# Performance work log

Hardware: AMD Instinct MI355X
Metric: run time of the kernel (lower is better)

The kernel has to match this reference:

```python
import jax, jax.numpy as jnp
import numpy as np

B, N, S = 32, 1000, 200
D, H, DK, FF, NL = 128, 8, 16, 512, 3
HK = H * DK


def _mha(x, Wq, Wk, Wv, Wo, bo):
    # x: [B, L, D]; manual multi-head attention matching the torch code
    Bv, L, _ = x.shape
    q = (x @ Wq).reshape(Bv, L, H, DK).transpose(0, 2, 1, 3)  # [B,H,L,dk]
    k = (x @ Wk).reshape(Bv, L, H, DK).transpose(0, 2, 1, 3)
    v = (x @ Wv).reshape(Bv, L, H, DK).transpose(0, 2, 1, 3)
    score = jnp.einsum('bhid,bhjd->bhij', q, k) / jnp.sqrt(jnp.asarray(DK, x.dtype))
    w = jax.nn.softmax(score, axis=-1)
    o = jnp.einsum('bhij,bhjd->bhid', w, v).transpose(0, 2, 1, 3).reshape(Bv, L, HK)
    return o @ Wo + bo


def _decoder_layer(x, Wq, Wk, Wv, Wo, bo, W1, b1, W2, b2):
    out1 = x + _mha(x, Wq, Wk, Wv, Wo, bo)
    ff = jax.nn.relu(out1 @ W1 + b1) @ W2 + b2
    return out1 + ff


def _forward(data, attention_bias, Wfirst, bfirst, Wlast, blast,
             Wq, Wk, Wv, Wo, bo, W1, b1, W2, b2, Wfin, bfin, sel):
    Bv, Np, Dm = data.shape
    Sn = sel.shape[1]
    bidx = jnp.arange(Bv)
    # _get_new_data: ordered list of unselected node indices, shape [B, N-S]
    mask = jnp.zeros((Bv, Np), bool).at[bidx[:, None], sel].set(True)
    vals = jnp.where(mask, Np, jnp.arange(Np)[None, :])
    unselect = jnp.sort(vals, axis=1)[:, : Np - Sn]            # [B, N-S]
    left = jnp.take_along_axis(data, unselect[:, :, None], axis=1)  # [B, N-S, D]
    # _get_encoding for first / last selected node
    first = data[bidx, sel[:, 0]]
    last = data[bidx, sel[:, -1]]
    ef = first @ Wfirst + bfirst
    el = last @ Wlast + blast
    out = jnp.concatenate([ef[:, None], left, el[:, None]], axis=1)  # [B, N-S+2, D]
    for i in range(Wq.shape[0]):
        out = _decoder_layer(out, Wq[i], Wk[i], Wv[i], Wo[i], bo[i],
                             W1[i], b1[i], W2[i], b2[i])
    logits = (out @ Wfin + bfin)[..., 0]                       # [B, N-S+2]
    # attention bias of current (last selected) node, gathered at unselected
    ab_cur = attention_bias[bidx, sel[:, -1]]                  # [B, N]
    ab_uns = jnp.take_along_axis(ab_cur, unselect, axis=1)     # [B, N-S]
    logits = logits.at[:, 1:-1].add(ab_uns)
    L = logits.shape[1]
    pos = jnp.arange(L)
    end_mask = (pos == 0) | (pos == L - 1)
    logits = jnp.where(end_mask[None, :], -jnp.inf, logits)
    props = jax.nn.softmax(logits, axis=-1)[:, 1:-1]           # [B, N-S]
    props = jnp.where(props <= 1e-5, props + 1e-7, props)
    # scatter back: selected positions -> -2, unselected -> props
    new_props = jnp.full((Bv, Np), -2.0, dtype=data.dtype)
    new_props = new_props.at[bidx[:, None], unselect].set(props)
    return new_props


def setup_inputs() -> dict:
    key = jax.random.key(0)
    ks = jax.random.split(key, 24)
    data = jax.random.normal(ks[0], (B, N, D), jnp.float32)
    # selected_node_list must contain unique indices per row (partial tour)
    sel = jax.vmap(lambda k: jax.random.permutation(k, N))(
        jax.random.split(ks[1], B))[:, :S].astype(jnp.int32)
    attention_bias = jax.random.normal(ks[2], (B, N, N), jnp.float32)

    def lin(k, shape, fan_in):
        return jax.random.normal(k, shape, jnp.float32) / np.float32(np.sqrt(fan_in))

    return dict(
        data=data,
        attention_bias=attention_bias,
        Wfirst=lin(ks[3], (D, D), D), bfirst=jnp.zeros((D,), jnp.float32),
        Wlast=lin(ks[4], (D, D), D), blast=jnp.zeros((D,), jnp.float32),
        Wq=lin(ks[5], (NL, D, HK), D),
        Wk=lin(ks[6], (NL, D, HK), D),
        Wv=lin(ks[7], (NL, D, HK), D),
        Wo=lin(ks[8], (NL, HK, D), HK), bo=jnp.zeros((NL, D), jnp.float32),
        W1=lin(ks[9], (NL, D, FF), D), b1=jnp.zeros((NL, FF), jnp.float32),
        W2=lin(ks[10], (NL, FF, D), FF), b2=jnp.zeros((NL, D), jnp.float32),
        Wfin=lin(ks[11], (D, 1), D), bfin=jnp.zeros((1,), jnp.float32),
        selected_node_list=sel,
    )


def reference(data, attention_bias, Wfirst, bfirst, Wlast, blast,
              Wq, Wk, Wv, Wo, bo, W1, b1, W2, b2, Wfin, bfin,
              selected_node_list):
    return _forward(data, attention_bias, Wfirst, bfirst, Wlast, blast,
                    Wq, Wk, Wv, Wo, bo, W1, b1, W2, b2, Wfin, bfin,
                    selected_node_list)
```

## Files before the change

kernel.cpp:

```cpp
#include <hip/hip_runtime.h>
#include <hip/hip_bf16.h>
#include <math.h>

#define NB 32
#define NN 1000
#define SS 200
#define DD 128
#define HH 8
#define DKK 16
#define FFD 512
#define NLAYER 3
#define LQ 802
#define LPAD 832
#define NPADK (LPAD - LQ)
#define MROWS (NB*LQ)
#define NBLK64 (MROWS/64)
#define NQT 26
#define NQT64 13
#define HSTR 516
#define TSTR 132
#define QSCALE 0.3606737602f

typedef __attribute__((ext_vector_type(8))) short short8;
typedef __attribute__((ext_vector_type(4))) short short4v;
typedef __attribute__((ext_vector_type(16))) float f32x16;
typedef __attribute__((ext_vector_type(2))) unsigned int uint2v;

static __device__ __forceinline__ unsigned short f2bf(float x) {
  union { float f; unsigned int u; } v; v.f = x;
  unsigned int r = v.u + 0x7fff + ((v.u >> 16) & 1);
  return (unsigned short)(r >> 16);
}

static __device__ __forceinline__ unsigned short f2bf1(float x) {
  unsigned int r;
  asm("v_cvt_pk_bf16_f32 %0, %1, 0" : "=v"(r) : "v"(x));
  return (unsigned short)r;
}

static __device__ __forceinline__ unsigned int cvtpk_bf16(float lo, float hi) {
  unsigned int r;
  asm("v_cvt_pk_bf16_f32 %0, %1, %2" : "=v"(r) : "v"(lo), "v"(hi));
  return r;
}

static __device__ __forceinline__ float max3f(float a, float b, float c) {
  float r;
  asm("v_max3_f32 %0, %1, %2, %3" : "=v"(r) : "v"(a), "v"(b), "v"(c));
  return r;
}

static __device__ __forceinline__ float exp2n(float x) {
  float r;
  asm("v_exp_f32 %0, %1" : "=v"(r) : "v"(x));
  return r;
}

static __device__ __forceinline__ uint2v pls(unsigned int a, unsigned int b) {
  return __builtin_amdgcn_permlane32_swap(a, b, false, false);
}
static __device__ __forceinline__ unsigned int fu(float x){ return __float_as_uint(x); }
static __device__ __forceinline__ float uf(unsigned int x){ return __uint_as_float(x); }

#define WCH 196608
__global__ __launch_bounds__(256) void k_wconv(const float* __restrict__ Wq, const float* __restrict__ Wk,
                       const float* __restrict__ Wv, const float* __restrict__ Wo,
                       const float* __restrict__ W1, const float* __restrict__ W2,
                       unsigned short* __restrict__ WtQKV, unsigned short* __restrict__ Wot,
                       unsigned short* __restrict__ W1t, unsigned short* __restrict__ W2t) {
  int e = blockIdx.x*256 + threadIdx.x;
  if (e >= 3*WCH) return;
  int layer = e / WCH, r = e - layer*WCH;
  if (r < 49152) {
    int n = r >> 7, k = r & 127;
    int sect = n >> 7, nn = n & 127;
    const float* W = (sect == 0) ? Wq : (sect == 1) ? Wk : Wv;
    WtQKV[layer*49152 + r] = f2bf1(W[layer*16384 + k*128 + nn]);
  } else if (r < 65536) {
    int r2 = r - 49152;
    int n = r2 >> 7, k = r2 & 127;
    Wot[layer*16384 + r2] = f2bf1(Wo[layer*16384 + k*128 + n]);
  } else if (r < 131072) {
    int r2 = r - 65536;
    int n = r2 >> 7, k = r2 & 127;
    W1t[layer*65536 + r2] = f2bf1(W1[layer*65536 + k*512 + n]);
  } else {
    int r2 = r - 131072;
    int n = r2 >> 9, k = r2 & 511;
    W2t[layer*65536 + r2] = f2bf1(W2[layer*65536 + k*128 + n]);
  }
}

__global__ __launch_bounds__(1024) void k_unselect(const int* __restrict__ sel,
                                                   int* __restrict__ unselect,
                                                   int* __restrict__ pos) {
  int b = blockIdx.x;
  int n = threadIdx.x;
  __shared__ unsigned char fl[1024];
  __shared__ int wsum[16];
  fl[n] = (n < NN) ? 1 : 0;
  __syncthreads();
  if (n < SS) fl[sel[b*SS + n]] = 0;
  __syncthreads();
  int flag = fl[n];
  unsigned long long m = __ballot(flag);
  int lane = n & 63, w = n >> 6;
  int pre = __popcll(m & ((1ULL << lane) - 1ULL));
  if (lane == 63) wsum[w] = pre + flag;
  __syncthreads();
  int off = 0;
  #pragma unroll
  for (int i = 0; i < 16; ++i) off += (i < w) ? wsum[i] : 0;
  if (n < NN) {
    if (flag) {
      int j = off + pre;
      unselect[b*800 + j] = n;
      pos[b*NN + n] = j + 1;
    } else {
      pos[b*NN + n] = -1;
    }
  }
}

__global__ __launch_bounds__(128) void k_embed_ends(const float* __restrict__ data,
                       const int* __restrict__ sel,
                       const float* __restrict__ Wfirst, const float* __restrict__ bfirst,
                       const float* __restrict__ Wlast, const float* __restrict__ blast,
                       float* __restrict__ X, unsigned short* __restrict__ Xbf) {
  int which = blockIdx.x, b = blockIdx.y, d = threadIdx.x;
  int l = (which == 0) ? 0 : LQ-1;
  __shared__ float xr[DD];
  int src = sel[b*SS + (which == 0 ? 0 : SS-1)];
  const float* W    = (which == 0) ? Wfirst : Wlast;
  const float* bias = (which == 0) ? bfirst : blast;
  xr[d] = data[((size_t)b*NN + src)*DD + d];
  __syncthreads();
  float acc = bias[d];
  #pragma unroll 4
  for (int k = 0; k < DD; ++k) acc += xr[k] * W[k*DD + d];
  size_t off = ((size_t)(b*LQ + l))*DD + d;
  X[off] = acc;
  Xbf[off] = f2bf1(acc);
}

__global__ __launch_bounds__(256) void k_embed_mid(const float* __restrict__ data,
                       const int* __restrict__ unselect,
                       float* __restrict__ X, unsigned short* __restrict__ Xbf) {
  int e = blockIdx.x*256 + threadIdx.x;
  int r = e >> 5;
  int c4 = (e & 31) * 4;
  int b = r / 800, j = r - b*800;
  int nidx = unselect[r];
  const float4 v = *(const float4*)&data[((size_t)b*NN + nidx)*DD + c4];
  size_t off = ((size_t)(b*LQ + 1 + j))*DD + c4;
  *(float4*)&X[off] = v;
  unsigned int lo = cvtpk_bf16(v.x, v.y);
  unsigned int hi = cvtpk_bf16(v.z, v.w);
  unsigned long long pk8 = ((unsigned long long)hi << 32) | (unsigned long long)lo;
  *(unsigned long long*)&Xbf[off] = pk8;
}

__global__ __launch_bounds__(256) void k_qkv_mfma(const unsigned short* __restrict__ Xbf,
                       const unsigned short* __restrict__ Wt,
                       unsigned short* __restrict__ Qb, unsigned short* __restrict__ Kb,
                       unsigned short* __restrict__ Vb) {
  int row0 = blockIdx.x * 64;
  int t = threadIdx.x, wave = t >> 6, lane = t & 63;
  int col = lane & 31, half = lane >> 5;
  int b0 = row0 / LQ;
  int l00 = row0 - b0*LQ;
  int split = LQ - l00;
  short8 a[2][8];
  const unsigned short* xb = Xbf + (size_t)(row0 + col)*DD + half*8;
  #pragma unroll
  for (int mi = 0; mi < 2; ++mi)
    #pragma unroll
    for (int s = 0; s < 8; ++s)
      a[mi][s] = *(const short8*)(xb + (size_t)mi*32*DD + s*16);
  #pragma unroll
  for (int nn = 0; nn < 3; ++nn) {
    int ni = wave*3 + nn;
    short8 bfr[8];
    const unsigned short* wb = Wt + (size_t)(ni*32 + col)*DD + half*8;
    #pragma unroll
    for (int s = 0; s < 8; ++s) bfr[s] = *(const short8*)(wb + s*16);
    f32x16 acc0 = {0.f,0.f,0.f,0.f,0.f,0.f,0.f,0.f,0.f,0.f,0.f,0.f,0.f,0.f,0.f,0.f};
    f32x16 acc1 = {0.f,0.f,0.f,0.f,0.f,0.f,0.f,0.f,0.f,0.f,0.f,0.f,0.f,0.f,0.f,0.f};
    #pragma unroll
    for (int s = 0; s < 8; ++s) {
      acc0 = __builtin_amdgcn_mfma_f32_32x32x16_bf16(a[0][s], bfr[s], acc0, 0, 0, 0);
      acc1 = __builtin_amdgcn_mfma_f32_32x32x16_bf16(a[1][s], bfr[s], acc1, 0, 0, 0);
    }
    int n = ni*32 + col;
    int sect = n >> 7, nc = n & 127;
    int h = nc >> 4, d = nc & 15;
    #pragma unroll
    for (int mi = 0; mi < 2; ++mi) {
      const f32x16& acc = mi ? acc1 : acc0;
      #pragma unroll
      for (int r = 0; r < 16; ++r) {
        int ml = mi*32 + (r&3) + 8*(r>>2) + 4*half;
        int over = (ml >= split);
        int b_ = b0 + over;
        int l  = over ? (ml - split) : (l00 + ml);
        size_t bh = (size_t)(b_*HH + h);
        float v = acc[r];
        if (sect == 0)      Qb[(bh*LPAD + l)*DKK + d] = f2bf1(v * QSCALE);
        else if (sect == 1) Kb[(bh*LPAD + l)*DKK + d] = f2bf1(v);
        else                Vb[(bh*LPAD + l)*DKK + d] = f2bf1(v);
      }
    }
  }
}

__global__ __launch_bounds__(256) void k_vt(const unsigned short* __restrict__ Vb,
                                            unsigned short* __restrict__ Vt,
                                            unsigned short* __restrict__ Kb) {
  __shared__ unsigned short Lt[16][72];
  int l0 = blockIdx.x * 64;
  int bh = blockIdx.y;
  int t = threadIdx.x;
  int l = t >> 2, d4 = (t & 3) * 4;
  ushort4 v = {0,0,0,0};
  if (l0 + l < LQ) v = *(const ushort4*)&Vb[((size_t)bh*LPAD + l0 + l)*DKK + d4];
  Lt[d4+0][l] = v.x; Lt[d4+1][l] = v.y; Lt[d4+2][l] = v.z; Lt[d4+3][l] = v.w;
  __syncthreads();
  int dk = t >> 4, lq = (t & 15)*4;
  ushort4 o;
  o.x = Lt[dk][lq]; o.y = Lt[dk][lq+1]; o.z = Lt[dk][lq+2]; o.w = Lt[dk][lq+3];
  *(ushort4*)&Vt[((size_t)bh*DKK + dk)*LPAD + l0 + lq] = o;
  if (blockIdx.x == 12 && t < 240)
    ((unsigned int*)&Kb[((size_t)bh*LPAD + LQ)*DKK])[t] = 0u;
}

__global__ __launch_bounds__(256) void k_attn3(const unsigned short* __restrict__ Q,
                       const unsigned short* __restrict__ K,
                       const unsigned short* __restrict__ Vt,
                       unsigned short* __restrict__ Obf) {
  int bid = blockIdx.x;
  int g = bid & 7, i = bid >> 3;
  int bhg = i / NQT64, qt = i - bhg*NQT64;
  int bh = bhg*8 + g;
  int b = bh >> 3, h = bh & 7;
  int q0 = qt*64;
  size_t bhL = (size_t)bh * LPAD;
  int t = threadIdx.x;
  int wave = t >> 6, lane = t & 63;
  int col = lane & 31;
  int half = lane >> 5;

  __shared__ float mw[2][4][32];
  __shared__ float sw[2][4][32];
  __shared__ float sfin[2][32];
  __shared__ float ored[2][4][16][32];
  __shared__ float osum[2][32][17];

  uint2v pr = pls(1000u + (unsigned)lane, 2000u + (unsigned)lane);
  bool case1 = (__builtin_amdgcn_readfirstlane((int)pr.x) >= 2000);

  int q0c = q0 + col;      if (q0c > LQ-1) q0c = LQ-1;
  int q1c = q0 + 32 + col; if (q1c > LQ-1) q1c = LQ-1;
  short8 bQ0 = *(const short8*)&Q[(bhL + q0c)*DKK + half*8];
  short8 bQ1 = *(const short8*)&Q[(bhL + q1c)*DKK + half*8];

  f32x16 oacc0 = {0.f,0.f,0.f,0.f,0.f,0.f,0.f,0.f,0.f,0.f,0.f,0.f,0.f,0.f,0.f,0.f};
  f32x16 oacc1 = oacc0;
  float runm0 = 0.f, runm1 = 0.f;
  bool act = false;

  short8 aV0 = {0,0,0,0,0,0,0,0};
  short8 aV1 = {0,0,0,0,0,0,0,0};
  if (col == 16) {
    union { unsigned int u[4]; short8 s8; } o;
    o.u[0] = o.u[1] = o.u[2] = o.u[3] = 0x3F803F80u;
    aV0 = o.s8; aV1 = o.s8;
  }

  for (int kt = wave; kt < NQT; kt += 4) {
    int key0 = kt*32;
    short8 aK = *(const short8*)&K[(bhL + key0 + col)*DKK + half*8];
    if (col < 16) {
      const unsigned short* vp = &Vt[((size_t)bh*DKK + col)*LPAD + key0 + half*8];
      aV0 = *(const short8*)vp;
      aV1 = *(const short8*)(vp + 16);
    }

    auto process = [&](const short8& bQ, f32x16& oacc, float& runm) {
      f32x16 c = {0.f,0.f,0.f,0.f,0.f,0.f,0.f,0.f,0.f,0.f,0.f,0.f,0.f,0.f,0.f,0.f};
      c = __builtin_amdgcn_mfma_f32_32x32x16_bf16(aK, bQ, c, 0, 0, 0);
      float m0 = max3f(c[0],  c[1],  c[2]);
      float m1 = max3f(c[3],  c[4],  c[5]);
      float m2 = max3f(c[6],  c[7],  c[8]);
      float m3 = max3f(c[9],  c[10], c[11]);
      float m4 = max3f(c[12], c[13], c[14]);
      float tm = fmaxf(max3f(m0, m1, m2), max3f(m3, m4, c[15]));
      if (!__all(tm <= runm + 80.0f)) {
        uint2v rr = pls(fu(tm), fu(tm));
        float tmp = max3f(tm, uf(rr.x), uf(rr.y));
        float mnew = fmaxf(runm, tmp);
        float sc = exp2n(runm - mnew);
        #pragma unroll
        for (int r = 0; r < 9; ++r) oacc[r] *= sc;
        runm = mnew;
        act = true;
      }
      float p[16];
      if (act) {
        #pragma unroll
        for (int r = 0; r < 16; ++r) p[r] = exp2n(c[r] - runm);
      } else {
        #pragma unroll
        for (int r = 0; r < 16; ++r) p[r] = exp2n(c[r]);
      }
      unsigned int pk[8];
      #pragma unroll
      for (int j = 0; j < 8; ++j) pk[j] = cvtpk_bf16(p[2*j], p[2*j+1]);
      unsigned int fAx, fAy, fAz, fAw, fBx, fBy, fBz, fBw;
      if (case1) {
        uint2v r0 = pls(pk[2], pk[0]); fAz = r0.x; fAx = r0.y;
        uint2v r1 = pls(pk[3], pk[1]); fAw = r1.x; fAy = r1.y;
        uint2v r2 = pls(pk[6], pk[4]); fBz = r2.x; fBx = r2.y;
        uint2v r3 = pls(pk[7], pk[5]); fBw = r3.x; fBy = r3.y;
      } else {
        uint2v r0 = pls(pk[0], pk[2]); fAx = r0.x; fAz = r0.y;
        uint2v r1 = pls(pk[1], pk[3]); fAy = r1.x; fAw = r1.y;
        uint2v r2 = pls(pk[4], pk[6]); fBx = r2.x; fBz = r2.y;
        uint2v r3 = pls(pk[5], pk[7]); fBy = r3.x; fBw = r3.y;
      }
      union { unsigned int u[4]; short8 s8; } fA, fB;
      fA.u[0] = fAx; fA.u[1] = fAy; fA.u[2] = fAz; fA.u[3] = fAw;
      fB.u[0] = fBx; fB.u[1] = fBy; fB.u[2] = fBz; fB.u[3] = fBw;
      oacc = __builtin_amdgcn_mfma_f32_32x32x16_bf16(aV0, fA.s8, oacc, 0, 0, 0);
      oacc = __builtin_amdgcn_mfma_f32_32x32x16_bf16(aV1, fB.s8, oacc, 0, 0, 0);
    };
    process(bQ0, oacc0, runm0);
    process(bQ1, oacc1, runm1);
  }

  if (half == 0) {
    mw[0][wave][col] = runm0;  sw[0][wave][col] = oacc0[8];
    mw[1][wave][col] = runm1;  sw[1][wave][col] = oacc1[8];
  }
  __syncthreads();
  #pragma unroll
  for (int u = 0; u < 2; ++u) {
    float M = fmaxf(fmaxf(mw[u][0][col], mw[u][1][col]), fmaxf(mw[u][2][col], mw[u][3][col]));
    float S = sw[u][0][col]*exp2n(mw[u][0][col]-M) + sw[u][1][col]*exp2n(mw[u][1][col]-M)
            + sw[u][2][col]*exp2n(mw[u][2][col]-M) + sw[u][3][col]*exp2n(mw[u][3][col]-M);
    float runm = u ? runm1 : runm0;
    float fw = exp2n(runm - M);
    const f32x16& oacc = u ? oacc1 : oacc0;
    #pragma unroll
    for (int r = 0; r < 8; ++r) {
      int dv = (r&3) + 8*(r>>2) + 4*half;
      ored[u][wave][dv][col] = oacc[r] * fw;
    }
    if (wave == 0 && half == 0)
      sfin[u][col] = S - (float)NPADK * exp2n(-M);
  }
  __syncthreads();
  {
    int qq = t & 31, dv0 = t >> 5;
    #pragma unroll
    for (int u = 0; u < 2; ++u)
      #pragma unroll
      for (int k = 0; k < 2; ++k) {
        int dv = dv0 + 8*k;
        osum[u][qq][dv] = ored[u][0][dv][qq] + ored[u][1][dv][qq]
                        + ored[u][2][dv][qq] + ored[u][3][dv][qq];
      }
  }
  __syncthreads();
  {
    int qs = t >> 3, c2 = (t & 7)*2;
    #pragma unroll
    for (int u = 0; u < 2; ++u) {
      int q = q0 + u*32 + qs;
      if (q < LQ) {
        float invS = 1.f / sfin[u][qs];
        unsigned int pkv = cvtpk_bf16(osum[u][qs][c2] * invS, osum[u][qs][c2+1] * invS);
        *(unsigned int*)&Obf[((size_t)(b*LQ + q))*DD + h*DKK + c2] = pkv;
      }
    }
  }
}

__global__ __launch_bounds__(256) void k_pff(const unsigned short* __restrict__ Obf,
        const unsigned short* __restrict__ Wot, const float* __restrict__ bo,
        const unsigned short* __restrict__ W1t, const float* __restrict__ b1,
        const unsigned short* __restrict__ W2t, const float* __restrict__ b2,
        float* __restrict__ X, unsigned short* __restrict__ Xbf) {
  __shared__ __align__(16) unsigned short LDSU[64 * HSTR];
  unsigned short* T  = LDSU;
  unsigned short* Hs = LDSU;
  int row0 = blockIdx.x * 64;
  int t = threadIdx.x, wave = t >> 6, lane = t & 63;
  int col = lane & 31, half = lane >> 5;
  int n = wave*32 + col;
  float res[2][16];
  {
    short8 a[2][8];
    const unsigned short* ob = Obf + (size_t)(row0 + col)*DD + half*8;
    #pragma unroll
    for (int mi = 0; mi < 2; ++mi)
      #pragma unroll
      for (int s = 0; s < 8; ++s)
        a[mi][s] = *(const short8*)(ob + (size_t)mi*32*DD + s*16);
    short8 bfr[8];
    const unsigned short* wb = Wot + (size_t)n*DD + half*8;
    #pragma unroll
    for (int s = 0; s < 8; ++s) bfr[s] = *(const short8*)(wb + s*16);
    f32x16 acc0 = {0.f,0.f,0.f,0.f,0.f,0.f,0.f,0.f,0.f,0.f,0.f,0.f,0.f,0.f,0.f,0.f};
    f32x16 acc1 = acc0;
    #pragma unroll
    for (int s = 0; s < 8; ++s) {
      acc0 = __builtin_amdgcn_mfma_f32_32x32x16_bf16(a[0][s], bfr[s], acc0, 0, 0, 0);
      acc1 = __builtin_amdgcn_mfma_f32_32x32x16_bf16(a[1][s], bfr[s], acc1, 0, 0, 0);
    }
    float bv = bo[n];
    #pragma unroll
    for (int mi = 0; mi < 2; ++mi) {
      const f32x16& acc = mi ? acc1 : acc0;
      #pragma unroll
      for (int r = 0; r < 16; ++r) {
        int ml = mi*32 + (r&3) + 8*(r>>2) + 4*half;
        size_t off = (size_t)(row0 + ml)*DD + n;
        res[mi][r] = X[off] + acc[r] + bv;
        T[ml*TSTR + n] = f2bf1(res[mi][r]);
      }
    }
  }
  __syncthreads();
  short8 aF[2][8];
  #pragma unroll
  for (int mi = 0; mi < 2; ++mi)
    #pragma unroll
    for (int s = 0; s < 8; ++s) {
      const unsigned short* tp = &T[(mi*32 + col)*TSTR + half*8 + s*16];
      union { short4v h[2]; short8 v; } u;
      u.h[0] = *(const short4v*)tp;
      u.h[1] = *(const short4v*)(tp + 4);
      aF[mi][s] = u.v;
    }
  __syncthreads();
  #pragma unroll
  for (int nn = 0; nn < 4; ++nn) {
    int ni = wave*4 + nn;
    short8 bfr[8];
    const unsigned short* wb = W1t + (size_t)(ni*32 + col)*DD + half*8;
    #pragma unroll
    for (int s = 0; s < 8; ++s) bfr[s] = *(const short8*)(wb + s*16);
    f32x16 acc0 = {0.f,0.f,0.f,0.f,0.f,0.f,0.f,0.f,0.f,0.f,0.f,0.f,0.f,0.f,0.f,0.f};
    f32x16 acc1 = acc0;
    #pragma unroll
    for (int s = 0; s < 8; ++s) {
      acc0 = __builtin_amdgcn_mfma_f32_32x32x16_bf16(aF[0][s], bfr[s], acc0, 0, 0, 0);
      acc1 = __builtin_amdgcn_mfma_f32_32x32x16_bf16(aF[1][s], bfr[s], acc1, 0, 0, 0);
    }
    int nf = ni*32 + col;
    float bv = b1[nf];
    #pragma unroll
    for (int mi = 0; mi < 2; ++mi) {
      const f32x16& acc = mi ? acc1 : acc0;
      #pragma unroll
      for (int r = 0; r < 16; ++r) {
        int ml = mi*32 + (r&3) + 8*(r>>2) + 4*half;
        Hs[ml*HSTR + nf] = f2bf1(fmaxf(acc[r] + bv, 0.f));
      }
    }
  }
  __syncthreads();
  f32x16 acc0 = {0.f,0.f,0.f,0.f,0.f,0.f,0.f,0.f,0.f,0.f,0.f,0.f,0.f,0.f,0.f,0.f};
  f32x16 acc1 = acc0;
  const unsigned short* w2b = W2t + (size_t)n*FFD + half*8;
  #pragma unroll 4
  for (int s = 0; s < 32; ++s) {
    int ko = s*16 + half*8;
    union { short4v h[2]; short8 v; } h0, h1;
    const unsigned short* hp0 = &Hs[col*HSTR + ko];
    const unsigned short* hp1 = &Hs[(32 + col)*HSTR + ko];
    h0.h[0] = *(const short4v*)hp0;  h0.h[1] = *(const short4v*)(hp0 + 4);
    h1.h[0] = *(const short4v*)hp1;  h1.h[1] = *(const short4v*)(hp1 + 4);
    short8 bfr = *(const short8*)(w2b + s*16);
    acc0 = __builtin_amdgcn_mfma_f32_32x32x16_bf16(h0.v, bfr, acc0, 0, 0, 0);
    acc1 = __builtin_amdgcn_mfma_f32_32x32x16_bf16(h1.v, bfr, acc1, 0, 0, 0);
  }
  float bv = b2[n];
  #pragma unroll
  for (int mi = 0; mi < 2; ++mi) {
    const f32x16& acc = mi ? acc1 : acc0;
    #pragma unroll
    for (int r = 0; r < 16; ++r) {
      int ml = mi*32 + (r&3) + 8*(r>>2) + 4*half;
      size_t off = (size_t)(row0 + ml)*DD + n;
      float v = res[mi][r] + acc[r] + bv;
      X[off] = v;
      Xbf[off] = f2bf1(v);
    }
  }
}

__global__ __launch_bounds__(256) void k_logits(const float* __restrict__ X,
                        const float* __restrict__ Wfin, const float* __restrict__ bfin,
                        float* __restrict__ logits) {
  int t = threadIdx.x, wave = t >> 6, lane = t & 63;
  int row = blockIdx.x*4 + wave;
  float2 xv = *(const float2*)&X[(size_t)row*DD + lane*2];
  float2 wv = *(const float2*)&Wfin[lane*2];
  float v = xv.x*wv.x + xv.y*wv.y;
  #pragma unroll
  for (int off = 32; off > 0; off >>= 1) v += __shfl_down(v, off);
  if (lane == 0) logits[row] = v + bfin[0];
}

__global__ __launch_bounds__(256) void k_final(const float* __restrict__ logits,
                       const float* __restrict__ AB, const int* __restrict__ sel,
                       const int* __restrict__ unselect, const int* __restrict__ pos,
                       float* __restrict__ out) {
  int b = blockIdx.x, t = threadIdx.x;
  __shared__ float sl[800];
  __shared__ float red[256];
  int lastsel = sel[b*SS + SS-1];
  const float* abrow = AB + ((size_t)b*NN + lastsel)*NN;
  for (int j = t; j < 800; j += 256)
    sl[j] = logits[b*LQ + j + 1] + abrow[unselect[b*800 + j]];
  __syncthreads();
  float lm = -INFINITY;
  for (int j = t; j < 800; j += 256) lm = fmaxf(lm, sl[j]);
  red[t] = lm;
  __syncthreads();
  for (int s = 128; s > 0; s >>= 1) {
    if (t < s) red[t] = fmaxf(red[t], red[t+s]);
    __syncthreads();
  }
  float m = red[0];
  __syncthreads();
  float ls = 0.f;
  for (int j = t; j < 800; j += 256) ls += __expf(sl[j] - m);
  red[t] = ls;
  __syncthreads();
  for (int s = 128; s > 0; s >>= 1) {
    if (t < s) red[t] += red[t+s];
    __syncthreads();
  }
  float inv = 1.f / red[0];
  for (int n = t; n < NN; n += 256) {
    int p1 = pos[b*NN + n];
    float v = -2.0f;
    if (p1 >= 0) {
      float p = __expf(sl[p1-1] - m) * inv;
      if (p <= 1e-5f) p += 1e-7f;
      v = p;
    }
    out[(size_t)b*NN + n] = v;
  }
}

extern "C" void kernel_launch(void* const* d_in, const int* in_sizes, int n_in,
                              void* d_out, int out_size, void* d_ws, size_t ws_size,
                              hipStream_t stream) {
  const float* data   = (const float*)d_in[0];
  const float* AB     = (const float*)d_in[1];
  const float* Wfirst = (const float*)d_in[2];
  const float* bfirst = (const float*)d_in[3];
  const float* Wlast  = (const float*)d_in[4];
  const float* blast  = (const float*)d_in[5];
  const float* Wq     = (const float*)d_in[6];
  const float* Wk     = (const float*)d_in[7];
  const float* Wv     = (const float*)d_in[8];
  const float* Wo     = (const float*)d_in[9];
  const float* bo     = (const float*)d_in[10];
  const float* W1     = (const float*)d_in[11];
  const float* b1     = (const float*)d_in[12];
  const float* W2     = (const float*)d_in[13];
  const float* b2     = (const float*)d_in[14];
  const float* Wfin   = (const float*)d_in[15];
  const float* bfin   = (const float*)d_in[16];
  const int*   sel    = (const int*)d_in[17];
  float* out = (float*)d_out;
  (void)in_sizes; (void)n_in; (void)out_size; (void)ws_size;

  char* ws = (char*)d_ws;
  const size_t NELT = (size_t)MROWS * DD;
  const size_t KVELT = (size_t)NB*HH*LPAD*DKK;
  int*   UNSEL = (int*)ws;
  int*   POS   = (int*)(ws + 102400);
  float* X     = (float*)(ws + 230400);
  unsigned short* Xbf = (unsigned short*)(X + NELT);
  unsigned short* Ob  = Xbf + NELT;
  unsigned short* Qb  = Ob + NELT;
  unsigned short* Kb  = Qb + KVELT;
  unsigned short* Vb  = Kb + KVELT;
  unsigned short* Vt  = Vb + KVELT;
  unsigned short* WtQKV = Vt + KVELT;
  unsigned short* Wot = WtQKV + (size_t)NLAYER*384*128;
  unsigned short* W1t = Wot + (size_t)NLAYER*128*128;
  unsigned short* W2t = W1t + (size_t)NLAYER*512*128;
  float* LOG = (float*)(W2t + (size_t)NLAYER*128*512);

  k_wconv<<<(3*WCH + 255)/256, 256, 0, stream>>>(Wq, Wk, Wv, Wo, W1, W2, WtQKV, Wot, W1t, W2t);
  k_unselect<<<NB, 1024, 0, stream>>>(sel, UNSEL, POS);
  k_embed_ends<<<dim3(2, NB), 128, 0, stream>>>(data, sel, Wfirst, bfirst, Wlast, blast, X, Xbf);
  k_embed_mid<<<3200, 256, 0, stream>>>(data, UNSEL, X, Xbf);
  for (int i = 0; i < NLAYER; ++i) {
    k_qkv_mfma<<<NBLK64, 256, 0, stream>>>(Xbf, WtQKV + (size_t)i*384*128, Qb, Kb, Vb);
    k_vt<<<dim3(13, NB*HH), 256, 0, stream>>>(Vb, Vt, Kb);
    k_attn3<<<NQT64*HH*NB, 256, 0, stream>>>(Qb, Kb, Vt, Ob);
    k_pff<<<NBLK64, 256, 0, stream>>>(Ob, Wot + (size_t)i*128*128, bo + (size_t)i*DD,
                                      W1t + (size_t)i*512*128, b1 + (size_t)i*FFD,
                                      W2t + (size_t)i*128*512, b2 + (size_t)i*DD, X, Xbf);
  }
  k_logits<<<MROWS/4, 256, 0, stream>>>(X, Wfin, bfin, LOG);
  k_final<<<NB, 256, 0, stream>>>(LOG, AB, sel, UNSEL, POS, out);
}
```

Baseline: 528.5 us.

## Write V transposed directly from QKV GEMM and fold logits into final kernel

The QKV projection kernel now writes V straight into the transposed Vt layout using packed bf16 pairs, so the separate k_vt transpose kernel and the intermediate Vb buffer are removed. Padding zeroing for K and Vt moves into a one-time k_padzero kernel. The final logits dot product is merged into k_final, which drops the k_logits launch and the logits buffer. The cost is that k_final now does per-row 128-element dot products with only 32 blocks, and the Vt stores are strided scattered 4-byte writes.

Result: no change. 534.0 us (+1.0%).

```diff
diff --git a/kernel.cpp b/kernel.cpp
--- a/kernel.cpp
+++ b/kernel.cpp
@@ -91,6 +91,20 @@
   }
 }
 
+__global__ __launch_bounds__(256) void k_padzero(unsigned short* __restrict__ Kb,
+                                                 unsigned short* __restrict__ Vt) {
+  int e = blockIdx.x*256 + threadIdx.x;
+  if (e < 61440) {
+    int bh = e / 240, r = e - bh*240;
+    ((unsigned int*)&Kb[((size_t)bh*LPAD + LQ)*DKK])[r] = 0u;
+  } else {
+    int e2 = e - 61440;
+    int bh = e2 / 240, r = e2 - bh*240;
+    int d = r / 15, li = r - d*15;
+    ((unsigned int*)&Vt[((size_t)bh*DKK + d)*LPAD + LQ])[li] = 0u;
+  }
+}
+
 __global__ __launch_bounds__(1024) void k_unselect(const int* __restrict__ sel,
                                                    int* __restrict__ unselect,
                                                    int* __restrict__ pos) {
@@ -163,7 +177,7 @@
 __global__ __launch_bounds__(256) void k_qkv_mfma(const unsigned short* __restrict__ Xbf,
                        const unsigned short* __restrict__ Wt,
                        unsigned short* __restrict__ Qb, unsigned short* __restrict__ Kb,
-                       unsigned short* __restrict__ Vb) {
+                       unsigned short* __restrict__ Vt) {
   int row0 = blockIdx.x * 64;
   int t = threadIdx.x, wave = t >> 6, lane = t & 63;
   int col = lane & 31, half = lane >> 5;
@@ -194,43 +208,39 @@
     int n = ni*32 + col;
     int sect = n >> 7, nc = n & 127;
     int h = nc >> 4, d = nc & 15;
-    #pragma unroll
-    for (int mi = 0; mi < 2; ++mi) {
-      const f32x16& acc = mi ? acc1 : acc0;
+    if (sect < 2) {
       #pragma unroll
-      for (int r = 0; r < 16; ++r) {
-        int ml = mi*32 + (r&3) + 8*(r>>2) + 4*half;
-        int over = (ml >= split);
-        int b_ = b0 + over;
-        int l  = over ? (ml - split) : (l00 + ml);
-        size_t bh = (size_t)(b_*HH + h);
-        float v = acc[r];
-        if (sect == 0)      Qb[(bh*LPAD + l)*DKK + d] = f2bf1(v * QSCALE);
-        else if (sect == 1) Kb[(bh*LPAD + l)*DKK + d] = f2bf1(v);
-        else                Vb[(bh*LPAD + l)*DKK + d] = f2bf1(v);
-      }
-    }
-  }
-}
-
-__global__ __launch_bounds__(256) void k_vt(const unsigned short* __restrict__ Vb,
-                                            unsigned short* __restrict__ Vt,
-                                            unsigned short* __restrict__ Kb) {
-  __shared__ unsigned short Lt[16][72];
-  int l0 = blockIdx.x * 64;
-  int bh = blockIdx.y;
-  int t = threadIdx.x;
-  int l = t >> 2, d4 = (t & 3) * 4;
-  ushort4 v = {0,0,0,0};
-  if (l0 + l < LQ) v = *(const ushort4*)&Vb[((size_t)bh*LPAD + l0 + l)*DKK + d4];
-  Lt[d4+0][l] = v.x; Lt[d4+1][l] = v.y; Lt[d4+2][l] = v.z; Lt[d4+3][l] = v.w;
-  __syncthreads();
-  int dk = t >> 4, lq = (t & 15)*4;
-  ushort4 o;
-  o.x = Lt[dk][lq]; o.y = Lt[dk][lq+1]; o.z = Lt[dk][lq+2]; o.w = Lt[dk][lq+3];
-  *(ushort4*)&Vt[((size_t)bh*DKK + dk)*LPAD + l0 + lq] = o;
-  if (blockIdx.x == 12 && t < 240)
-    ((unsigned int*)&Kb[((size_t)bh*LPAD + LQ)*DKK])[t] = 0u;
+      for (int mi = 0; mi < 2; ++mi) {
+        const f32x16& acc = mi ? acc1 : acc0;
+        #pragma unroll
+        for (int r = 0; r < 16; ++r) {
+          int ml = mi*32 + (r&3) + 8*(r>>2) + 4*half;
+          int over = (ml >= split);
+          int b_ = b0 + over;
+          int l  = over ? (ml - split) : (l00 + ml);
+          size_t bh = (size_t)(b_*HH + h);
+          float v = acc[r];
+          if (sect == 0) Qb[(bh*LPAD + l)*DKK + d] = f2bf1(v * QSCALE);
+          else           Kb[(bh*LPAD + l)*DKK + d] = f2bf1(v);
+        }
+      }
+    } else {
+      #pragma unroll
+      for (int mi = 0; mi < 2; ++mi) {
+        const f32x16& acc = mi ? acc1 : acc0;
+        #pragma unroll
+        for (int pj = 0; pj < 8; ++pj) {
+          int j = pj >> 1, pi = pj & 1;
+          int mlp = mi*32 + 8*j + 4*half + 2*pi;
+          int over = (mlp >= split);
+          int b_ = b0 + over;
+          int l  = over ? (mlp - split) : (l00 + mlp);
+          unsigned int w = cvtpk_bf16(acc[4*j + 2*pi], acc[4*j + 2*pi + 1]);
+          *(unsigned int*)&Vt[((size_t)(b_*HH + h)*DKK + d)*LPAD + l] = w;
+        }
+      }
+    }
+  }
 }
 
 __global__ __launch_bounds__(256) void k_attn3(const unsigned short* __restrict__ Q,
@@ -500,30 +510,30 @@
   }
 }
 
-__global__ __launch_bounds__(256) void k_logits(const float* __restrict__ X,
-                        const float* __restrict__ Wfin, const float* __restrict__ bfin,
-                        float* __restrict__ logits) {
-  int t = threadIdx.x, wave = t >> 6, lane = t & 63;
-  int row = blockIdx.x*4 + wave;
-  float2 xv = *(const float2*)&X[(size_t)row*DD + lane*2];
-  float2 wv = *(const float2*)&Wfin[lane*2];
-  float v = xv.x*wv.x + xv.y*wv.y;
-  #pragma unroll
-  for (int off = 32; off > 0; off >>= 1) v += __shfl_down(v, off);
-  if (lane == 0) logits[row] = v + bfin[0];
-}
-
-__global__ __launch_bounds__(256) void k_final(const float* __restrict__ logits,
+__global__ __launch_bounds__(256) void k_final(const float* __restrict__ X,
+                       const float* __restrict__ Wfin, const float* __restrict__ bfin,
                        const float* __restrict__ AB, const int* __restrict__ sel,
                        const int* __restrict__ unselect, const int* __restrict__ pos,
                        float* __restrict__ out) {
   int b = blockIdx.x, t = threadIdx.x;
   __shared__ float sl[800];
   __shared__ float red[256];
+  __shared__ float wf[DD];
+  if (t < DD) wf[t] = Wfin[t];
   int lastsel = sel[b*SS + SS-1];
   const float* abrow = AB + ((size_t)b*NN + lastsel)*NN;
-  for (int j = t; j < 800; j += 256)
-    sl[j] = logits[b*LQ + j + 1] + abrow[unselect[b*800 + j]];
+  float bias = bfin[0];
+  __syncthreads();
+  for (int j = t; j < 800; j += 256) {
+    const float* xr = &X[((size_t)(b*LQ + 1 + j))*DD];
+    float acc = 0.f;
+    #pragma unroll 8
+    for (int k = 0; k < DD; k += 4) {
+      float4 xv = *(const float4*)&xr[k];
+      acc += xv.x*wf[k] + xv.y*wf[k+1] + xv.z*wf[k+2] + xv.w*wf[k+3];
+    }
+    sl[j] = acc + bias + abrow[unselect[b*800 + j]];
+  }
   __syncthreads();
   float lm = -INFINITY;
   for (int j = t; j < 800; j += 256) lm = fmaxf(lm, sl[j]);
@@ -590,26 +600,23 @@
   unsigned short* Ob  = Xbf + NELT;
   unsigned short* Qb  = Ob + NELT;
   unsigned short* Kb  = Qb + KVELT;
-  unsigned short* Vb  = Kb + KVELT;
-  unsigned short* Vt  = Vb + KVELT;
+  unsigned short* Vt  = Kb + KVELT;
   unsigned short* WtQKV = Vt + KVELT;
   unsigned short* Wot = WtQKV + (size_t)NLAYER*384*128;
   unsigned short* W1t = Wot + (size_t)NLAYER*128*128;
   unsigned short* W2t = W1t + (size_t)NLAYER*512*128;
-  float* LOG = (float*)(W2t + (size_t)NLAYER*128*512);
 
   k_wconv<<<(3*WCH + 255)/256, 256, 0, stream>>>(Wq, Wk, Wv, Wo, W1, W2, WtQKV, Wot, W1t, W2t);
+  k_padzero<<<480, 256, 0, stream>>>(Kb, Vt);
   k_unselect<<<NB, 1024, 0, stream>>>(sel, UNSEL, POS);
   k_embed_ends<<<dim3(2, NB), 128, 0, stream>>>(data, sel, Wfirst, bfirst, Wlast, blast, X, Xbf);
   k_embed_mid<<<3200, 256, 0, stream>>>(data, UNSEL, X, Xbf);
   for (int i = 0; i < NLAYER; ++i) {
-    k_qkv_mfma<<<NBLK64, 256, 0, stream>>>(Xbf, WtQKV + (size_t)i*384*128, Qb, Kb, Vb);
-    k_vt<<<dim3(13, NB*HH), 256, 0, stream>>>(Vb, Vt, Kb);
+    k_qkv_mfma<<<NBLK64, 256, 0, stream>>>(Xbf, WtQKV + (size_t)i*384*128, Qb, Kb, Vt);
     k_attn3<<<NQT64*HH*NB, 256, 0, stream>>>(Qb, Kb, Vt, Ob);
     k_pff<<<NBLK64, 256, 0, stream>>>(Ob, Wot + (size_t)i*128*128, bo + (size_t)i*DD,
                                       W1t + (size_t)i*512*128, b1 + (size_t)i*FFD,
                                       W2t + (size_t)i*128*512, b2 + (size_t)i*DD, X, Xbf);
   }
-  k_logits<<<MROWS/4, 256, 0, stream>>>(X, Wfin, bfin, LOG);
-  k_final<<<NB, 256, 0, stream>>>(LOG, AB, sel, UNSEL, POS, out);
-}
+  k_final<<<NB, 256, 0, stream>>>(X, Wfin, bfin, AB, sel, UNSEL, POS, out);
+}
```
